# Kernel optimization log

Hardware: AMD Instinct MI355X
Metric: run time of the kernel (lower is better)

The kernel has to match this reference:

```python
import jax, jax.numpy as jnp
import numpy as np

N_NODES = 100000
N_GRAPHS = 64


def gcn_layer(x, src, dst, W, b, n):
    # GCNConv: h = x @ W; out_i = sum_j norm_ij * h_j (+ self loop), + bias
    h = x @ W
    deg = jax.ops.segment_sum(jnp.ones(src.shape[0], x.dtype), dst, num_segments=n)
    dinv = jnp.where(deg > 0, jax.lax.rsqrt(deg), 0.0)
    norm = dinv[src] * dinv[dst]                      # [E+N]
    agg = jax.ops.segment_sum(h[src] * norm[:, None], dst, num_segments=n)
    return agg + b


def setup_inputs() -> dict:
    key = jax.random.key(0)
    ks = jax.random.split(key, 12)
    nfeat, nhid, nclass = 128, 64, 10
    E = 1600000
    x = jax.random.normal(ks[0], (N_NODES, nfeat), dtype=jnp.float32)
    edge_index = jax.random.randint(ks[1], (2, E), 0, N_NODES, dtype=jnp.int64)
    batch = jnp.sort(jax.random.randint(ks[2], (N_NODES,), 0, N_GRAPHS, dtype=jnp.int64))
    def w(k, fi, fo):
        return jax.random.normal(k, (fi, fo), dtype=jnp.float32) / np.sqrt(fi)
    return {
        "x": x, "edge_index": edge_index, "batch": batch,
        "W1": w(ks[3], nfeat, nhid), "b1": jnp.zeros((nhid,), jnp.float32),
        "W2": w(ks[4], nhid, nhid), "b2": jnp.zeros((nhid,), jnp.float32),
        "W3": w(ks[5], nhid, nhid), "b3": jnp.zeros((nhid,), jnp.float32),
        "Wl": w(ks[6], nhid, nclass), "bl": jnp.zeros((nclass,), jnp.float32),
    }


def reference(x, edge_index, batch, W1, b1, W2, b2, W3, b3, Wl, bl):
    n = x.shape[0]
    loop = jnp.arange(n, dtype=edge_index.dtype)
    src = jnp.concatenate([edge_index[0], loop])   # self-loops appended
    dst = jnp.concatenate([edge_index[1], loop])
    h = x  # eval mode: dropout is identity; use_bn=False
    for W, b in ((W1, b1), (W2, b2), (W3, b3)):
        h = jax.nn.relu(gcn_layer(h, src, dst, W, b, n))
    # global mean pool per graph
    sums = jax.ops.segment_sum(h, batch, num_segments=N_GRAPHS)
    cnts = jax.ops.segment_sum(jnp.ones((n,), h.dtype), batch, num_segments=N_GRAPHS)
    pooled = sums / jnp.maximum(cnts, 1.0)[:, None]   # [G, nhid]
    logits = pooled @ Wl + bl
    return jax.nn.softmax(logits, axis=1)
```

## Files before the change

kernel.cpp:

```cpp
#include <hip/hip_runtime.h>
#include <math.h>


__device__ __forceinline__ unsigned short f2bf(float f) {
    unsigned int u = __float_as_uint(f);
    u += 0x7fffu + ((u >> 16) & 1u);
    return (unsigned short)(u >> 16);
}
__device__ __forceinline__ float bf2f(unsigned short u) {
    return __uint_as_float((unsigned int)u << 16);
}
__device__ __forceinline__ float bflo(unsigned int u) {
    return __uint_as_float(u << 16);
}
__device__ __forceinline__ float bfhi(unsigned int u) {
    return __uint_as_float(u & 0xffff0000u);
}

__global__ void zero_kernel(float* __restrict__ a, int n) {
    int i = blockIdx.x * 256 + threadIdx.x;
    if (i < n) a[i] = 0.f;
}


__global__ __launch_bounds__(256) void hist_kernel(const int* __restrict__ dst,
                                                   int* __restrict__ counts,
                                                   int E, int P, int C) {
    __shared__ int hist[256];
    int t = threadIdx.x, b = blockIdx.x;
    if (t < P) hist[t] = 0;
    __syncthreads();
    int beg = b * C, end = min(E, beg + C);
    for (int e = beg + t; e < end; e += 256)
        atomicAdd(&hist[dst[e] >> 9], 1);
    __syncthreads();
    if (t < P) counts[t * 256 + b] = hist[t];
}

__global__ __launch_bounds__(256) void pscan_kernel(const int* __restrict__ counts,
                                                    int* __restrict__ pbase,
                                                    int* __restrict__ rowptr,
                                                    int P, int N) {
    __shared__ int s[256];
    int t = threadIdx.x;
    int v = 0;
    if (t < P)
        for (int b = 0; b < 256; ++b) v += counts[t * 256 + b];
    s[t] = v;
    __syncthreads();
    for (int off = 1; off < 256; off <<= 1) {
        int u = (t >= off) ? s[t - off] : 0;
        __syncthreads();
        s[t] += u;
        __syncthreads();
    }
    if (t < P) pbase[t] = s[t] - v;
    if (t == 255) { pbase[P] = s[255]; rowptr[N] = s[255]; }
}

__global__ __launch_bounds__(256) void offs_kernel(const int* __restrict__ counts,
                                                   const int* __restrict__ pbase,
                                                   int* __restrict__ offs) {
    __shared__ int s[256];
    int t = threadIdx.x, p = blockIdx.x;
    int v = counts[p * 256 + t];
    s[t] = v;
    __syncthreads();
    for (int off = 1; off < 256; off <<= 1) {
        int u = (t >= off) ? s[t - off] : 0;
        __syncthreads();
        s[t] += u;
        __syncthreads();
    }
    offs[p * 256 + t] = pbase[p] + s[t] - v;
}

__global__ __launch_bounds__(256) void bin_kernel(const int* __restrict__ src,
                                                  const int* __restrict__ dst,
                                                  const int* __restrict__ offs,
                                                  unsigned int* __restrict__ binned,
                                                  int E, int P, int C) {
    __shared__ int cur[256];
    int t = threadIdx.x, b = blockIdx.x;
    if (t < P) cur[t] = offs[t * 256 + b];
    __syncthreads();
    int beg = b * C, end = min(E, beg + C);
    for (int e = beg + t; e < end; e += 256) {
        int d = dst[e], s = src[e];
        int pos = atomicAdd(&cur[d >> 9], 1);
        binned[pos] = ((unsigned int)s << 9) | (unsigned int)(d & 511);
    }
}

__global__ __launch_bounds__(512) void lsortA_kernel(const unsigned int* __restrict__ binned,
                                                     const int* __restrict__ pbase,
                                                     int* __restrict__ rowptr,
                                                     float* __restrict__ dinv, int N) {
    __shared__ int ldeg[512];
    __shared__ int s[512];
    int t = threadIdx.x, p = blockIdx.x;
    int lo = p << 9;
    ldeg[t] = 0;
    __syncthreads();
    int eBeg = pbase[p], eEnd = pbase[p + 1];
    for (int j = eBeg + t; j < eEnd; j += 512)
        atomicAdd(&ldeg[binned[j] & 511u], 1);
    __syncthreads();
    int v = ldeg[t];
    s[t] = v;
    __syncthreads();
    for (int off = 1; off < 512; off <<= 1) {
        int u = (t >= off) ? s[t - off] : 0;
        __syncthreads();
        s[t] += u;
        __syncthreads();
    }
    if (lo + t < N) {
        rowptr[lo + t] = eBeg + s[t] - v;
        dinv[lo + t] = rsqrtf((float)(v + 1));
    }
}

__global__ __launch_bounds__(256) void lsortB_kernel(const unsigned int* __restrict__ binned,
                                                     const int* __restrict__ pbase,
                                                     const int* __restrict__ rowptr,
                                                     const float* __restrict__ dinv,
                                                     float2* __restrict__ csrw, int N) {
    __shared__ int cur[512];
    __shared__ float sdi[512];
    int t = threadIdx.x, p = blockIdx.x;
    int lo = p << 9, hi = min(N, lo + 512);
    for (int i = t; i < hi - lo; i += 256) {
        cur[i] = rowptr[lo + i];
        sdi[i] = dinv[lo + i];
    }
    __syncthreads();
    int eBeg = pbase[p], eEnd = pbase[p + 1];
    for (int j = eBeg + t; j < eEnd; j += 256) {
        unsigned int v = binned[j];
        int s = (int)(v >> 9);
        int dl = (int)(v & 511u);
        int pos = atomicAdd(&cur[dl], 1);
        csrw[pos] = make_float2(__int_as_float(s << 7), dinv[s] * sdi[dl]);
    }
}

template <int FIN, bool RELU>
__global__ __launch_bounds__(256) void gemm_kernel(const float* __restrict__ X,
                                                   const float* __restrict__ W,
                                                   unsigned short* __restrict__ H, int N) {
    constexpr int FINP = FIN + 4;
    __shared__ float sW[FIN * 64];
    __shared__ float sX[64 * FINP];
    int tid = threadIdx.x;
    for (int i = tid * 4; i < FIN * 64; i += 1024)
        *(float4*)&sW[i] = *(const float4*)&W[i];
    int rowBase = blockIdx.x * 64;
    for (int i = tid * 4; i < 64 * FIN; i += 1024) {
        int r = i / FIN, c = i - r * FIN;
        int gr = rowBase + r;
        float4 v = make_float4(0.f, 0.f, 0.f, 0.f);
        if (gr < N) {
            v = *(const float4*)&X[(long)gr * FIN + c];
            if (RELU) {
                v.x = fmaxf(v.x, 0.f); v.y = fmaxf(v.y, 0.f);
                v.z = fmaxf(v.z, 0.f); v.w = fmaxf(v.w, 0.f);
            }
        }
        *(float4*)&sX[r * FINP + c] = v;
    }
    __syncthreads();
    int tx = tid & 15;
    int ty = tid >> 4;
    float acc[4][4];
#pragma unroll
    for (int rr = 0; rr < 4; ++rr)
#pragma unroll
        for (int cc = 0; cc < 4; ++cc) acc[rr][cc] = 0.f;
#pragma unroll 1
    for (int k = 0; k < FIN; k += 4) {
        float xr[4][4], wr[4][4];
#pragma unroll
        for (int rr = 0; rr < 4; ++rr)
            *(float4*)xr[rr] = *(const float4*)&sX[(ty + 16 * rr) * FINP + k];
#pragma unroll
        for (int kk = 0; kk < 4; ++kk)
            *(float4*)wr[kk] = *(const float4*)&sW[(k + kk) * 64 + 4 * tx];
#pragma unroll
        for (int rr = 0; rr < 4; ++rr)
#pragma unroll
            for (int kk = 0; kk < 4; ++kk)
#pragma unroll
                for (int cc = 0; cc < 4; ++cc)
                    acc[rr][cc] = fmaf(xr[rr][kk], wr[kk][cc], acc[rr][cc]);
    }
#pragma unroll
    for (int rr = 0; rr < 4; ++rr) {
        int gr = rowBase + ty + 16 * rr;
        if (gr < N) {
            ushort4 o;
            o.x = f2bf(acc[rr][0]); o.y = f2bf(acc[rr][1]);
            o.z = f2bf(acc[rr][2]); o.w = f2bf(acc[rr][3]);
            *(ushort4*)&H[(long)gr * 64 + 4 * tx] = o;
        }
    }
}

__global__ __launch_bounds__(256) void gather_kernel(const float2* __restrict__ csrw,
                                                     const int* __restrict__ rowptr,
                                                     const unsigned short* __restrict__ h,
                                                     const float* __restrict__ dinv,
                                                     const float* __restrict__ b,
                                                     float* __restrict__ agg, int N) {
    int node = (blockIdx.x * 256 + threadIdx.x) >> 6;
    int lane = threadIdx.x & 63;
    if (node >= N) return;
    int g = lane >> 3;
    int f = lane & 7;
    int fo = f * 16;
    int beg = rowptr[node], end = rowptr[node + 1];
    float di = dinv[node];

    float acc[8];
#pragma unroll
    for (int k = 0; k < 8; ++k) acc[k] = 0.f;

    if (g == 0) {
        uint4 us = *(const uint4*)((const char*)h + ((size_t)node << 7) + fo);
        float s2 = di * di;
        float4 bv0 = *(const float4*)&b[f * 8];
        float4 bv1 = *(const float4*)&b[f * 8 + 4];
        acc[0] = fmaf(s2, bflo(us.x), bv0.x);
        acc[1] = fmaf(s2, bfhi(us.x), bv0.y);
        acc[2] = fmaf(s2, bflo(us.y), bv0.z);
        acc[3] = fmaf(s2, bfhi(us.y), bv0.w);
        acc[4] = fmaf(s2, bflo(us.z), bv1.x);
        acc[5] = fmaf(s2, bfhi(us.z), bv1.y);
        acc[6] = fmaf(s2, bflo(us.w), bv1.z);
        acc[7] = fmaf(s2, bfhi(us.w), bv1.w);
    }

    const char* hb = (const char*)h;
    for (int e = beg; e < end; e += 32) {
        float2 c[4];
        float w[4];
#pragma unroll
        for (int q = 0; q < 4; ++q) {
            int idx = e + 8 * q + g;
            c[q] = csrw[idx < end ? idx : end - 1];
            w[q] = idx < end ? 1.f : 0.f;
        }
        uint4 u[4];
#pragma unroll
        for (int q = 0; q < 4; ++q)
            u[q] = *(const uint4*)(hb + __float_as_int(c[q].x) + fo);
#pragma unroll
        for (int q = 0; q < 4; ++q) {
            float wq = w[q] * c[q].y;
            acc[0] = fmaf(wq, bflo(u[q].x), acc[0]);
            acc[1] = fmaf(wq, bfhi(u[q].x), acc[1]);
            acc[2] = fmaf(wq, bflo(u[q].y), acc[2]);
            acc[3] = fmaf(wq, bfhi(u[q].y), acc[3]);
            acc[4] = fmaf(wq, bflo(u[q].z), acc[4]);
            acc[5] = fmaf(wq, bfhi(u[q].z), acc[5]);
            acc[6] = fmaf(wq, bflo(u[q].w), acc[6]);
            acc[7] = fmaf(wq, bfhi(u[q].w), acc[7]);
        }
    }

#pragma unroll
    for (int k = 0; k < 8; ++k) {
        float v = acc[k];
        v += __shfl_xor(v, 8);
        v += __shfl_xor(v, 16);
        v += __shfl_xor(v, 32);
        acc[k] = v;
    }
    if (g == 0) {
        float* ap = &agg[((size_t)node << 6) + f * 8];
        *(float4*)ap = make_float4(acc[0], acc[1], acc[2], acc[3]);
        *(float4*)(ap + 4) = make_float4(acc[4], acc[5], acc[6], acc[7]);
    }
}

__global__ __launch_bounds__(256) void pool_kernel(const float* __restrict__ h,
                                                   const int* __restrict__ batch,
                                                   float* __restrict__ sums,
                                                   float* __restrict__ cnts, int N) {
    int col = threadIdx.x & 63;
    int wave = threadIdx.x >> 6;
    int base = blockIdx.x * 256 + wave * 64;
    float acc = 0.f, cnt = 0.f;
    int curg = -1;
    for (int j = 0; j < 64; ++j) {
        int node = base + j;
        if (node >= N) break;
        int g = batch[node];
        if (g != curg) {
            if (curg >= 0) {
                atomicAdd(&sums[curg * 64 + col], acc);
                if (col == 0) atomicAdd(&cnts[curg], cnt);
            }
            acc = 0.f; cnt = 0.f;
            curg = g;
        }
        acc += fmaxf(h[(long)node * 64 + col], 0.f);
        cnt += 1.f;
    }
    if (curg >= 0) {
        atomicAdd(&sums[curg * 64 + col], acc);
        if (col == 0) atomicAdd(&cnts[curg], cnt);
    }
}

__global__ void final_kernel(const float* __restrict__ sums, const float* __restrict__ cnts,
                             const float* __restrict__ Wl, const float* __restrict__ bl,
                             float* __restrict__ out, int G) {
    int g = blockIdx.x * blockDim.x + threadIdx.x;
    if (g >= G) return;
    float inv = 1.0f / fmaxf(cnts[g], 1.0f);
    float logits[10];
#pragma unroll
    for (int k = 0; k < 10; ++k) logits[k] = bl[k];
    for (int c = 0; c < 64; ++c) {
        float p = sums[g * 64 + c] * inv;
#pragma unroll
        for (int k = 0; k < 10; ++k) logits[k] = fmaf(p, Wl[c * 10 + k], logits[k]);
    }
    float m = logits[0];
#pragma unroll
    for (int k = 1; k < 10; ++k) m = fmaxf(m, logits[k]);
    float se = 0.f;
#pragma unroll
    for (int k = 0; k < 10; ++k) { logits[k] = expf(logits[k] - m); se += logits[k]; }
    float is = 1.0f / se;
#pragma unroll
    for (int k = 0; k < 10; ++k) out[g * 10 + k] = logits[k] * is;
}

extern "C" void kernel_launch(void* const* d_in, const int* in_sizes, int n_in,
                              void* d_out, int out_size, void* d_ws, size_t ws_size,
                              hipStream_t stream) {
    const float* x    = (const float*)d_in[0];
    const int* edges  = (const int*)d_in[1];
    const int* batch  = (const int*)d_in[2];
    const float* W1   = (const float*)d_in[3];
    const float* b1   = (const float*)d_in[4];
    const float* W2   = (const float*)d_in[5];
    const float* b2   = (const float*)d_in[6];
    const float* W3   = (const float*)d_in[7];
    const float* b3   = (const float*)d_in[8];
    const float* Wl   = (const float*)d_in[9];
    const float* bl   = (const float*)d_in[10];

    const int N = in_sizes[0] / 128;
    const int E = in_sizes[1] / 2;
    const int G = out_size / 10;
    const int* src = edges;
    const int* dst = edges + E;

    float* ws     = (float*)d_ws;
    unsigned short* h = (unsigned short*)ws;
    float* agg    = ws + (size_t)N * 64;
    unsigned int* binned = (unsigned int*)ws;
    float2* csrw  = (float2*)(ws + (size_t)2 * N * 64);
    float* dinv   = ws + (size_t)2 * N * 64 + (size_t)2 * E;
    int*   rowptr = (int*)(dinv + N);
    int*   counts = rowptr + N + 1;
    int*   offs   = counts + 256 * 256;
    int*   pbase  = offs + 256 * 256;
    float* sums   = (float*)(pbase + 257);
    float* cnts   = sums + (size_t)G * 64;

    const int gemmGrid = (N + 63) / 64;
    const int gatherGrid = (N + 3) / 4;
    const int P = (N + 511) >> 9;
    const int C = (E + 255) / 256;

    hist_kernel<<<256, 256, 0, stream>>>(dst, counts, E, P, C);
    pscan_kernel<<<1, 256, 0, stream>>>(counts, pbase, rowptr, P, N);
    offs_kernel<<<P, 256, 0, stream>>>(counts, pbase, offs);
    bin_kernel<<<256, 256, 0, stream>>>(src, dst, offs, binned, E, P, C);
    lsortA_kernel<<<P, 512, 0, stream>>>(binned, pbase, rowptr, dinv, N);
    lsortB_kernel<<<P, 256, 0, stream>>>(binned, pbase, rowptr, dinv, csrw, N);

    gemm_kernel<128, false><<<gemmGrid, 256, 0, stream>>>(x, W1, h, N);
    gather_kernel<<<gatherGrid, 256, 0, stream>>>(csrw, rowptr, h, dinv, b1, agg, N);

    gemm_kernel<64, true><<<gemmGrid, 256, 0, stream>>>(agg, W2, h, N);
    gather_kernel<<<gatherGrid, 256, 0, stream>>>(csrw, rowptr, h, dinv, b2, agg, N);

    gemm_kernel<64, true><<<gemmGrid, 256, 0, stream>>>(agg, W3, h, N);
    gather_kernel<<<gatherGrid, 256, 0, stream>>>(csrw, rowptr, h, dinv, b3, agg, N);

    zero_kernel<<<(G * 65 + 255) / 256, 256, 0, stream>>>(sums, G * 65);
    pool_kernel<<<(N + 255) / 256, 256, 0, stream>>>(agg, batch, sums, cnts, N);
    final_kernel<<<1, 64, 0, stream>>>(sums, cnts, Wl, bl, (float*)d_out, G);
}
```

Before: 410.9 us.

## Use bf16 MFMA GEMMs and store layer activations as bf16 with fused ReLU

Replaces the fp32 LDS-tiled FMA GEMM with a bf16 MFMA 16x16x32 kernel that reads operands directly into registers, using weights pre-transposed and converted to bf16 by a new prep kernel. The gather kernel now applies ReLU and writes bf16 activations instead of fp32, which halves the aggregate traffic read by the next GEMM and by the pool kernel. This trades fp32 precision in the intermediate activations for fewer memory bytes and matrix-core throughput, and it adds one small extra launch.

```diff
diff --git a/kernel.cpp b/kernel.cpp
--- a/kernel.cpp
+++ b/kernel.cpp
@@ -1,6 +1,9 @@
 #include <hip/hip_runtime.h>
 #include <math.h>
 
+
+typedef __attribute__((ext_vector_type(8))) short bf16x8;
+typedef __attribute__((ext_vector_type(4))) float f32x4;
 
 __device__ __forceinline__ unsigned short f2bf(float f) {
     unsigned int u = __float_as_uint(f);
@@ -145,63 +148,70 @@
     }
 }
 
-template <int FIN, bool RELU>
-__global__ __launch_bounds__(256) void gemm_kernel(const float* __restrict__ X,
-                                                   const float* __restrict__ W,
-                                                   unsigned short* __restrict__ H, int N) {
-    constexpr int FINP = FIN + 4;
-    __shared__ float sW[FIN * 64];
-    __shared__ float sX[64 * FINP];
-    int tid = threadIdx.x;
-    for (int i = tid * 4; i < FIN * 64; i += 1024)
-        *(float4*)&sW[i] = *(const float4*)&W[i];
-    int rowBase = blockIdx.x * 64;
-    for (int i = tid * 4; i < 64 * FIN; i += 1024) {
-        int r = i / FIN, c = i - r * FIN;
-        int gr = rowBase + r;
-        float4 v = make_float4(0.f, 0.f, 0.f, 0.f);
-        if (gr < N) {
-            v = *(const float4*)&X[(long)gr * FIN + c];
-            if (RELU) {
-                v.x = fmaxf(v.x, 0.f); v.y = fmaxf(v.y, 0.f);
-                v.z = fmaxf(v.z, 0.f); v.w = fmaxf(v.w, 0.f);
-            }
+__global__ __launch_bounds__(256) void prepw_kernel(const float* __restrict__ W1,
+                                                    const float* __restrict__ W2,
+                                                    const float* __restrict__ W3,
+                                                    unsigned short* __restrict__ Wt1,
+                                                    unsigned short* __restrict__ Wt2,
+                                                    unsigned short* __restrict__ Wt3) {
+    int t = threadIdx.x, b = blockIdx.x;
+    const float* W = (b == 0) ? W1 : ((b == 1) ? W2 : W3);
+    unsigned short* Wt = (b == 0) ? Wt1 : ((b == 1) ? Wt2 : Wt3);
+    int K = (b == 0) ? 128 : 64;
+    int o = t & 63;
+    for (int k = t >> 6; k < K; k += 4)
+        Wt[o * K + k] = f2bf(W[k * 64 + o]);
+}
+
+template <int FIN, bool F32IN>
+__global__ __launch_bounds__(256) void gemm_mfma_kernel(const void* __restrict__ Xv,
+                                                        const unsigned short* __restrict__ Wt,
+                                                        unsigned short* __restrict__ H,
+                                                        int N) {
+    constexpr int KS = FIN / 32;
+    int wave = threadIdx.x >> 6;
+    int lane = threadIdx.x & 63;
+    int r = lane & 15, g = lane >> 4;
+    int node = blockIdx.x * 64 + wave * 16 + r;
+    int nodeL = min(node, N - 1);
+
+    bf16x8 afr[4][KS];
+#pragma unroll
+    for (int m = 0; m < 4; ++m)
+#pragma unroll
+        for (int s = 0; s < KS; ++s)
+            afr[m][s] = *(const bf16x8*)&Wt[(m * 16 + r) * FIN + s * 32 + g * 8];
+
+    f32x4 acc[4];
+#pragma unroll
+    for (int m = 0; m < 4; ++m) acc[m] = (f32x4){0.f, 0.f, 0.f, 0.f};
+
+#pragma unroll
+    for (int s = 0; s < KS; ++s) {
+        bf16x8 bfr;
+        if (F32IN) {
+            const float* X = (const float*)Xv + (size_t)nodeL * FIN + s * 32 + g * 8;
+            float4 lo = *(const float4*)X;
+            float4 hi = *(const float4*)(X + 4);
+            bfr[0] = (short)f2bf(lo.x); bfr[1] = (short)f2bf(lo.y);
+            bfr[2] = (short)f2bf(lo.z); bfr[3] = (short)f2bf(lo.w);
+            bfr[4] = (short)f2bf(hi.x); bfr[5] = (short)f2bf(hi.y);
+            bfr[6] = (short)f2bf(hi.z); bfr[7] = (short)f2bf(hi.w);
+        } else {
+            bfr = *(const bf16x8*)((const unsigned short*)Xv + (size_t)nodeL * FIN + s * 32 + g * 8);
         }
-        *(float4*)&sX[r * FINP + c] = v;
-    }
-    __syncthreads();
-    int tx = tid & 15;
-    int ty = tid >> 4;
-    float acc[4][4];
-#pragma unroll
-    for (int rr = 0; rr < 4; ++rr)
-#pragma unroll
-        for (int cc = 0; cc < 4; ++cc) acc[rr][cc] = 0.f;
-#pragma unroll 1
-    for (int k = 0; k < FIN; k += 4) {
-        float xr[4][4], wr[4][4];
-#pragma unroll
-        for (int rr = 0; rr < 4; ++rr)
-            *(float4*)xr[rr] = *(const float4*)&sX[(ty + 16 * rr) * FINP + k];
-#pragma unroll
-        for (int kk = 0; kk < 4; ++kk)
-            *(float4*)wr[kk] = *(const float4*)&sW[(k + kk) * 64 + 4 * tx];
-#pragma unroll
-        for (int rr = 0; rr < 4; ++rr)
-#pragma unroll
-            for (int kk = 0; kk < 4; ++kk)
-#pragma unroll
-                for (int cc = 0; cc < 4; ++cc)
-                    acc[rr][cc] = fmaf(xr[rr][kk], wr[kk][cc], acc[rr][cc]);
-    }
-#pragma unroll
-    for (int rr = 0; rr < 4; ++rr) {
-        int gr = rowBase + ty + 16 * rr;
-        if (gr < N) {
+#pragma unroll
+        for (int m = 0; m < 4; ++m)
+            acc[m] = __builtin_amdgcn_mfma_f32_16x16x32_bf16(afr[m][s], bfr, acc[m], 0, 0, 0);
+    }
+
+    if (node < N) {
+#pragma unroll
+        for (int m = 0; m < 4; ++m) {
             ushort4 o;
-            o.x = f2bf(acc[rr][0]); o.y = f2bf(acc[rr][1]);
-            o.z = f2bf(acc[rr][2]); o.w = f2bf(acc[rr][3]);
-            *(ushort4*)&H[(long)gr * 64 + 4 * tx] = o;
+            o.x = f2bf(acc[m][0]); o.y = f2bf(acc[m][1]);
+            o.z = f2bf(acc[m][2]); o.w = f2bf(acc[m][3]);
+            *(ushort4*)&H[(size_t)node * 64 + m * 16 + g * 4] = o;
         }
     }
 }
@@ -211,7 +221,7 @@
                                                      const unsigned short* __restrict__ h,
                                                      const float* __restrict__ dinv,
                                                      const float* __restrict__ b,
-                                                     float* __restrict__ agg, int N) {
+                                                     unsigned short* __restrict__ aggb, int N) {
     int node = (blockIdx.x * 256 + threadIdx.x) >> 6;
     int lane = threadIdx.x & 63;
     if (node >= N) return;
@@ -274,16 +284,19 @@
         v += __shfl_xor(v, 8);
         v += __shfl_xor(v, 16);
         v += __shfl_xor(v, 32);
-        acc[k] = v;
+        acc[k] = fmaxf(v, 0.f);
     }
     if (g == 0) {
-        float* ap = &agg[((size_t)node << 6) + f * 8];
-        *(float4*)ap = make_float4(acc[0], acc[1], acc[2], acc[3]);
-        *(float4*)(ap + 4) = make_float4(acc[4], acc[5], acc[6], acc[7]);
-    }
-}
-
-__global__ __launch_bounds__(256) void pool_kernel(const float* __restrict__ h,
+        uint4 o;
+        o.x = ((unsigned)f2bf(acc[1]) << 16) | f2bf(acc[0]);
+        o.y = ((unsigned)f2bf(acc[3]) << 16) | f2bf(acc[2]);
+        o.z = ((unsigned)f2bf(acc[5]) << 16) | f2bf(acc[4]);
+        o.w = ((unsigned)f2bf(acc[7]) << 16) | f2bf(acc[6]);
+        *(uint4*)&aggb[((size_t)node << 6) + f * 8] = o;
+    }
+}
+
+__global__ __launch_bounds__(256) void pool_kernel(const unsigned short* __restrict__ hb,
                                                    const int* __restrict__ batch,
                                                    float* __restrict__ sums,
                                                    float* __restrict__ cnts, int N) {
@@ -304,7 +317,7 @@
             acc = 0.f; cnt = 0.f;
             curg = g;
         }
-        acc += fmaxf(h[(long)node * 64 + col], 0.f);
+        acc += bf2f(hb[(size_t)node * 64 + col]);
         cnt += 1.f;
     }
     if (curg >= 0) {
@@ -361,7 +374,7 @@
 
     float* ws     = (float*)d_ws;
     unsigned short* h = (unsigned short*)ws;
-    float* agg    = ws + (size_t)N * 64;
+    unsigned short* aggb = (unsigned short*)(ws + (size_t)N * 64);
     unsigned int* binned = (unsigned int*)ws;
     float2* csrw  = (float2*)(ws + (size_t)2 * N * 64);
     float* dinv   = ws + (size_t)2 * N * 64 + (size_t)2 * E;
@@ -372,6 +385,12 @@
     float* sums   = (float*)(pbase + 257);
     float* cnts   = sums + (size_t)G * 64;
 
+    size_t cntOff = (size_t)2 * N * 64 + (size_t)2 * E + N + (N + 1);
+    size_t wtOff  = (cntOff + 3) & ~(size_t)3;
+    unsigned short* Wt1 = (unsigned short*)(ws + wtOff);
+    unsigned short* Wt2 = Wt1 + 64 * 128;
+    unsigned short* Wt3 = Wt2 + 64 * 64;
+
     const int gemmGrid = (N + 63) / 64;
     const int gatherGrid = (N + 3) / 4;
     const int P = (N + 511) >> 9;
@@ -380,20 +399,21 @@
     hist_kernel<<<256, 256, 0, stream>>>(dst, counts, E, P, C);
     pscan_kernel<<<1, 256, 0, stream>>>(counts, pbase, rowptr, P, N);
     offs_kernel<<<P, 256, 0, stream>>>(counts, pbase, offs);
+    prepw_kernel<<<3, 256, 0, stream>>>(W1, W2, W3, Wt1, Wt2, Wt3);
     bin_kernel<<<256, 256, 0, stream>>>(src, dst, offs, binned, E, P, C);
     lsortA_kernel<<<P, 512, 0, stream>>>(binned, pbase, rowptr, dinv, N);
     lsortB_kernel<<<P, 256, 0, stream>>>(binned, pbase, rowptr, dinv, csrw, N);
 
-    gemm_kernel<128, false><<<gemmGrid, 256, 0, stream>>>(x, W1, h, N);
-    gather_kernel<<<gatherGrid, 256, 0, stream>>>(csrw, rowptr, h, dinv, b1, agg, N);
-
-    gemm_kernel<64, true><<<gemmGrid, 256, 0, stream>>>(agg, W2, h, N);
-    gather_kernel<<<gatherGrid, 256, 0, stream>>>(csrw, rowptr, h, dinv, b2, agg, N);
-
-    gemm_kernel<64, true><<<gemmGrid, 256, 0, stream>>>(agg, W3, h, N);
-    gather_kernel<<<gatherGrid, 256, 0, stream>>>(csrw, rowptr, h, dinv, b3, agg, N);
+    gemm_mfma_kernel<128, true><<<gemmGrid, 256, 0, stream>>>(x, Wt1, h, N);
+    gather_kernel<<<gatherGrid, 256, 0, stream>>>(csrw, rowptr, h, dinv, b1, aggb, N);
+
+    gemm_mfma_kernel<64, false><<<gemmGrid, 256, 0, stream>>>(aggb, Wt2, h, N);
+    gather_kernel<<<gatherGrid, 256, 0, stream>>>(csrw, rowptr, h, dinv, b2, aggb, N);
+
+    gemm_mfma_kernel<64, false><<<gemmGrid, 256, 0, stream>>>(aggb, Wt3, h, N);
+    gather_kernel<<<gatherGrid, 256, 0, stream>>>(csrw, rowptr, h, dinv, b3, aggb, N);
 
     zero_kernel<<<(G * 65 + 255) / 256, 256, 0, stream>>>(sums, G * 65);
-    pool_kernel<<<(N + 255) / 256, 256, 0, stream>>>(agg, batch, sums, cnts, N);
+    pool_kernel<<<(N + 255) / 256, 256, 0, stream>>>(aggb, batch, sums, cnts, N);
     final_kernel<<<1, 64, 0, stream>>>(sums, cnts, Wl, bl, (float*)d_out, G);
 }
```

Result: faster. 393.8 us (-4.1%).
